# Optimization experiments

Hardware: AMD Instinct MI355X
Metric: run time of the kernel (lower is better)

The kernel has to match this reference:

```python
import jax, jax.numpy as jnp
import numpy as np
from jax.scipy.special import logsumexp

B, P, C, NOBJ = 32, 16384, 80, 50
THRESH = 0.5
NEGPOS = 3
VAR0, VAR1 = 0.1, 0.2


def setup_inputs() -> dict:
    key = jax.random.key(0)
    k1, k2, k3, k4, k5, k6, k7, k8 = jax.random.split(key, 8)
    loc_data = jax.random.normal(k1, (B, P, 4), dtype=jnp.float32)
    conf_data = jax.random.normal(k2, (B, P, C), dtype=jnp.float32)
    obj_data = jax.random.normal(k3, (B, P, 2), dtype=jnp.float32)
    # priors in (cx, cy, w, h) form, all in (0,1)
    cxcy = jax.random.uniform(k4, (P, 2), dtype=jnp.float32)
    wh = 0.05 + 0.45 * jax.random.uniform(k5, (P, 2), dtype=jnp.float32)
    priors = jnp.concatenate([cxcy, wh], axis=1)
    # targets: [xmin, ymin, xmax, ymax, label(1..C), weight]
    xy1 = 0.75 * jax.random.uniform(k6, (B, NOBJ, 2), dtype=jnp.float32)
    bwh = 0.02 + 0.23 * jax.random.uniform(k7, (B, NOBJ, 2), dtype=jnp.float32)
    lab = jax.random.randint(k8, (B, NOBJ, 1), 1, C + 1).astype(jnp.float32)
    wgt = 0.5 + 0.5 * jax.random.uniform(jax.random.fold_in(key, 99), (B, NOBJ, 1), dtype=jnp.float32)
    targets = jnp.concatenate([xy1, xy1 + bwh, lab, wgt], axis=-1)
    return {"loc_data": loc_data, "conf_data": conf_data, "obj_data": obj_data,
            "priors": priors, "targets": targets}


def point_form(p):
    return jnp.concatenate([p[:, :2] - p[:, 2:] / 2, p[:, :2] + p[:, 2:] / 2], axis=1)


def jaccard(a, b):  # a: [No,4] corner boxes, b: [Np,4] corner boxes
    lt = jnp.maximum(a[:, None, :2], b[None, :, :2])
    rb = jnp.minimum(a[:, None, 2:], b[None, :, 2:])
    wh = jnp.clip(rb - lt, 0.0)
    inter = wh[..., 0] * wh[..., 1]
    area_a = (a[:, 2] - a[:, 0]) * (a[:, 3] - a[:, 1])
    area_b = (b[:, 2] - b[:, 0]) * (b[:, 3] - b[:, 1])
    return inter / (area_a[:, None] + area_b[None, :] - inter)


def encode(matched, priors):
    g_cxcy = ((matched[:, :2] + matched[:, 2:]) / 2 - priors[:, :2]) / (VAR0 * priors[:, 2:])
    g_wh = jnp.log((matched[:, 2:] - matched[:, :2]) / priors[:, 2:]) / VAR1
    return jnp.concatenate([g_cxcy, g_wh], axis=1)


def match_one(truths, labels, priors):
    overlaps = jaccard(truths, point_form(priors))       # [No, Np]
    best_prior_idx = jnp.argmax(overlaps, axis=1)        # [No]
    best_truth_overlap = jnp.max(overlaps, axis=0)       # [Np]
    best_truth_idx = jnp.argmax(overlaps, axis=0)        # [Np]
    # ensure every GT keeps its best prior (overlap forced to 2)
    best_truth_overlap = best_truth_overlap.at[best_prior_idx].set(2.0)
    best_truth_idx = best_truth_idx.at[best_prior_idx].set(jnp.arange(truths.shape[0]))
    matched = truths[best_truth_idx]                     # [Np,4]
    lab = jnp.where(best_truth_overlap < THRESH, 0.0, labels[best_truth_idx, 0])
    w = labels[best_truth_idx, 1]
    loc = encode(matched, priors)
    return loc, jnp.stack([lab, w], axis=1), lab > 0


def _rank_desc(x):
    # rank of each entry in a descending per-row sort
    return jnp.argsort(jnp.argsort(-x, axis=1), axis=1)


def _ce(logits, tgt):
    return logsumexp(logits, axis=-1) - jnp.take_along_axis(logits, tgt[..., None], axis=-1)[..., 0]


def reference(loc_data, conf_data, obj_data, priors, targets):
    priors_c = jax.lax.stop_gradient(priors)
    targets_c = jax.lax.stop_gradient(targets)
    truths, labels = targets_c[:, :, :4], targets_c[:, :, 4:6]
    loc_t, conf_t, pos = jax.vmap(lambda t, l: match_one(t, l, priors_c))(truths, labels)
    nb, npri = pos.shape
    w = conf_t[:, :, 1]
    posf = pos.astype(loc_data.dtype)
    num_pos = (w * posf).sum(axis=1).astype(jnp.int32)           # weighted count, truncated
    num_neg = jnp.clip(NEGPOS * num_pos, None, npri - 1)

    # weighted smooth-L1 localization loss over positives
    d = loc_data - loc_t
    ad = jnp.abs(d)
    sl1 = jnp.where(ad < 1.0, 0.5 * d * d, ad - 0.5).sum(-1)     # [B,P]
    loss_l = jnp.sum(sl1 * w * posf)

    # combined objectness+class logits: [B,P,C+1]
    lse = logsumexp(conf_data, axis=-1, keepdims=True)
    logit = jnp.concatenate([obj_data[..., 0:1] + lse, obj_data[..., 1:2] + conf_data], axis=-1)
    tgt_c = conf_t[:, :, 0].astype(jnp.int32)
    ce_c = _ce(logit, tgt_c)                                     # [B,P]
    mine_c = jnp.where(pos, 0.0, jax.lax.stop_gradient(ce_c))
    neg_c = _rank_desc(mine_c) < num_neg[:, None]
    mask_c = pos | neg_c
    loss_c = jnp.sum(ce_c * w * mask_c)

    # objectness loss with its own hard-negative mining
    ce_o = _ce(obj_data, pos.astype(jnp.int32))
    mine_o = jnp.where(pos, 0.0, jax.lax.stop_gradient(ce_o))
    neg_o = _rank_desc(mine_o) < num_neg[:, None]
    mask_o = pos | neg_o
    loss_obj = jnp.sum(ce_o * w * mask_o)

    N = jnp.sum(w * posf)
    return loss_l / N, loss_c / N, loss_obj / N
```

## Files before the change

### kernel.cpp

```cpp
#include <hip/hip_runtime.h>
#include <cstdint>
#include <cstddef>

#define B_    32
#define P_    16384
#define C_    80
#define NOBJ_ 50
#define THRESH_ 0.5f

static constexpr size_t OFF_BP    = 1024;
static constexpr size_t OFF_MINEC = 16384;
static constexpr size_t SZ_BP32   = (size_t)B_ * P_ * 4;
static constexpr size_t OFF_MINEO = OFF_MINEC + SZ_BP32;
static constexpr size_t OFF_W     = OFF_MINEO + SZ_BP32;
static constexpr size_t OFF_POS   = OFF_W + SZ_BP32;
static constexpr size_t OFF_PMAIN = OFF_POS + (size_t)B_ * P_;
static constexpr size_t OFF_PSEL  = OFF_PMAIN + 2048 * 4 * 8;

__device__ __forceinline__ unsigned fkey(float f) {
    unsigned u = __float_as_uint(f);
    return (u & 0x80000000u) ? ~u : (u | 0x80000000u);
}

__device__ __forceinline__ void hist_add(unsigned bin, unsigned* hist) {
    int lane = threadIdx.x & 63;
    bool done = false;
    #pragma unroll
    for (int it = 0; it < 3; ++it) {
        unsigned long long active = __ballot(!done);
        if (!active) break;
        int leader = __ffsll((long long)active) - 1;
        unsigned lbin = __shfl(bin, leader);
        unsigned long long same = __ballot(!done && bin == lbin);
        if (!done && bin == lbin) {
            if (lane == leader) atomicAdd(&hist[bin], (unsigned)__popcll(same));
            done = true;
        }
    }
    if (!done) atomicAdd(&hist[bin], 1u);
}

__device__ double block_reduce_d(double v, double* sh, int nthreads) {
    int tid = threadIdx.x;
    sh[tid] = v; __syncthreads();
    for (int s = nthreads >> 1; s > 0; s >>= 1) {
        if (tid < s) sh[tid] += sh[tid + s];
        __syncthreads();
    }
    double r = sh[0]; __syncthreads();
    return r;
}

__global__ __launch_bounds__(256) void k_best_prior(
    const float* __restrict__ priors, const float* __restrict__ targets,
    int* __restrict__ bp)
{
    int t = blockIdx.x, b = blockIdx.y, tid = threadIdx.x;
    const float* tr = targets + (size_t)(b * NOBJ_ + t) * 6;
    float x1 = tr[0], y1 = tr[1], x2 = tr[2], y2 = tr[3];
    float areaA = (x2 - x1) * (y2 - y1);
    float best = -1.f; int bi = 0;
    for (int p = tid; p < P_; p += 256) {
        float4 pr = ((const float4*)priors)[p];
        float bx1 = pr.x - pr.z*0.5f, by1 = pr.y - pr.w*0.5f;
        float bx2 = pr.x + pr.z*0.5f, by2 = pr.y + pr.w*0.5f;
        float areaB = (bx2 - bx1) * (by2 - by1);
        float lx = fmaxf(x1, bx1), ly = fmaxf(y1, by1);
        float rx = fminf(x2, bx2), ry = fminf(y2, by2);
        float iw = fmaxf(rx - lx, 0.f), ih = fmaxf(ry - ly, 0.f);
        float inter = iw * ih;
        float iou = inter / (areaA + areaB - inter);
        if (iou > best) { best = iou; bi = p; }
    }
    __shared__ float sv[256];
    __shared__ int   si[256];
    sv[tid] = best; si[tid] = bi; __syncthreads();
    for (int s = 128; s > 0; s >>= 1) {
        if (tid < s) {
            if (sv[tid+s] > sv[tid] || (sv[tid+s] == sv[tid] && si[tid+s] < si[tid])) {
                sv[tid] = sv[tid+s]; si[tid] = si[tid+s];
            }
        }
        __syncthreads();
    }
    if (tid == 0) bp[b * NOBJ_ + t] = si[0];
}

__global__ __launch_bounds__(256) void k_main(
    const float* __restrict__ loc, const float* __restrict__ conf,
    const float* __restrict__ obj, const float* __restrict__ priors,
    const float* __restrict__ targets, const int* __restrict__ bp,
    float* __restrict__ mine_c, float* __restrict__ mine_o,
    float* __restrict__ wArr, uint8_t* __restrict__ posArr,
    double* __restrict__ pmain)
{
    int b = blockIdx.y;
    int row_base = blockIdx.x * 256;
    size_t base = (size_t)b * P_ + row_base;

    __shared__ float tg[NOBJ_ * 6];
    __shared__ float areaA[NOBJ_];
    __shared__ int   bpl[NOBJ_];
    __shared__ double wsum[4][4];
    for (int i = threadIdx.x; i < NOBJ_ * 6; i += 256) tg[i] = targets[(size_t)b * NOBJ_ * 6 + i];
    if (threadIdx.x < NOBJ_) bpl[threadIdx.x] = bp[b * NOBJ_ + threadIdx.x];
    __syncthreads();
    if (threadIdx.x < NOBJ_) {
        int t = threadIdx.x;
        areaA[t] = (tg[t*6+2] - tg[t*6+0]) * (tg[t*6+3] - tg[t*6+1]);
    }
    __syncthreads();

    int p = row_base + threadIdx.x;
    size_t ip = base + threadIdx.x;

    float4 prv = ((const float4*)priors)[p];
    float bx1 = prv.x - prv.z*0.5f, by1 = prv.y - prv.w*0.5f;
    float bx2 = prv.x + prv.z*0.5f, by2 = prv.y + prv.w*0.5f;
    float areaB = (bx2 - bx1) * (by2 - by1);
    float ov = -1.0f; int ti = 0;
    for (int t = 0; t < NOBJ_; ++t) {
        float lx = fmaxf(tg[t*6+0], bx1), ly = fmaxf(tg[t*6+1], by1);
        float rx = fminf(tg[t*6+2], bx2), ry = fminf(tg[t*6+3], by2);
        float iw = fmaxf(rx - lx, 0.f), ih = fmaxf(ry - ly, 0.f);
        float inter = iw * ih;
        float iou = inter / (areaA[t] + areaB - inter);
        if (iou > ov) { ov = iou; ti = t; }
    }
    for (int j = 0; j < NOBJ_; ++j) {
        if (bpl[j] == p) { ov = 2.0f; ti = j; }
    }

    float w  = tg[ti*6+5];
    bool pos = ov >= THRESH_;
    int  tgt = pos ? (int)tg[ti*6+4] : 0;

    float tx1 = tg[ti*6+0], ty1 = tg[ti*6+1], tx2 = tg[ti*6+2], ty2 = tg[ti*6+3];
    float gx = ((tx1 + tx2) * 0.5f - prv.x) / (0.1f * prv.z);
    float gy = ((ty1 + ty2) * 0.5f - prv.y) / (0.1f * prv.w);
    float gw = __logf((tx2 - tx1) / prv.z) * 5.0f;
    float gh = __logf((ty2 - ty1) / prv.w) * 5.0f;

    float4 l4 = ((const float4*)loc)[ip];
    float sl1 = 0.f;
    {
        float lrk[4] = {l4.x, l4.y, l4.z, l4.w};
        float g[4] = {gx, gy, gw, gh};
        #pragma unroll
        for (int k = 0; k < 4; ++k) {
            float d = lrk[k] - g[k];
            float ad = fabsf(d);
            sl1 += (ad < 1.0f) ? 0.5f * d * d : ad - 0.5f;
        }
    }

    float2 ob = ((const float2*)obj)[ip];
    float o0 = ob.x, o1 = ob.y;
    float mo = fmaxf(o0, o1);
    float lae = mo + __logf(__expf(o0 - mo) + __expf(o1 - mo));

    float ce_o = lae - (pos ? o1 : o0);
    float ce_c;
    if (tgt == 0) {
        ce_c = lae - o0;
    } else {
        const float4* cr = (const float4*)(conf + ip * C_);
        float m = -INFINITY;
        #pragma unroll 4
        for (int k = 0; k < C_/4; ++k) {
            float4 v = cr[k];
            m = fmaxf(m, fmaxf(fmaxf(v.x, v.y), fmaxf(v.z, v.w)));
        }
        float s = 0.f;
        #pragma unroll 4
        for (int k = 0; k < C_/4; ++k) {
            float4 v = cr[k];
            s += __expf(v.x - m) + __expf(v.y - m) + __expf(v.z - m) + __expf(v.w - m);
        }
        float lse = m + __logf(s);
        float ctgt = conf[ip * C_ + (tgt - 1)];
        ce_c = lse + lae - o1 - ctgt;
    }

    mine_c[ip] = pos ? 0.f : ce_c;
    mine_o[ip] = pos ? 0.f : ce_o;
    wArr[ip]   = w;
    posArr[ip] = pos ? 1 : 0;

    double v0 = pos ? (double)(sl1 * w)  : 0.0;
    double v1 = pos ? (double)(ce_c * w) : 0.0;
    double v2 = pos ? (double)(ce_o * w) : 0.0;
    double v3 = pos ? (double)w          : 0.0;

    #pragma unroll
    for (int d = 32; d; d >>= 1) {
        v0 += __shfl_xor(v0, d);
        v1 += __shfl_xor(v1, d);
        v2 += __shfl_xor(v2, d);
        v3 += __shfl_xor(v3, d);
    }
    int wid = threadIdx.x >> 6, lane = threadIdx.x & 63;
    if (lane == 0) { wsum[wid][0] = v0; wsum[wid][1] = v1; wsum[wid][2] = v2; wsum[wid][3] = v3; }
    __syncthreads();
    if (threadIdx.x == 0) {
        double t0 = 0, t1 = 0, t2 = 0, t3 = 0;
        #pragma unroll
        for (int i = 0; i < 4; ++i) { t0 += wsum[i][0]; t1 += wsum[i][1]; t2 += wsum[i][2]; t3 += wsum[i][3]; }
        size_t flat = (size_t)b * gridDim.x + blockIdx.x;
        pmain[flat*4+0] = t0; pmain[flat*4+1] = t1; pmain[flat*4+2] = t2; pmain[flat*4+3] = t3;
    }
}

#define SEL_T 1024
#define TIE_CAP 1024

__device__ __forceinline__ void suffix_scan_2048(unsigned* c, unsigned* wtot) {
    int tid = threadIdx.x;
    int lane = tid & 63, wid = tid >> 6;
    unsigned lo = c[2*tid], hi = c[2*tid+1];
    unsigned s_hi = hi;
    unsigned s_lo = lo + hi;
    unsigned tot = s_lo;
    unsigned run = tot;
    #pragma unroll
    for (int d = 1; d < 64; d <<= 1) {
        unsigned o = __shfl_down(run, d);
        if (lane + d < 64) run += o;
    }
    if (lane == 0) wtot[wid] = run;
    __syncthreads();
    unsigned woff = 0;
    #pragma unroll
    for (int w = 0; w < 16; ++w) if (w > wid) woff += wtot[w];
    unsigned base = woff + (run - tot);
    __syncthreads();
    c[2*tid]   = base + s_lo;
    c[2*tid+1] = base + s_hi;
    __syncthreads();
}

__device__ __forceinline__ void find_bin(unsigned* c, int K, int* s_bin, int* s_pre) {
    int tid = threadIdx.x;
    #pragma unroll
    for (int i = 0; i < 2; ++i) {
        int bb = tid + i * 1024;
        unsigned cb = c[bb];
        unsigned cn = (bb == 2047) ? 0u : c[bb + 1];
        if (cb >= (unsigned)K && cn < (unsigned)K) { *s_bin = bb; *s_pre = (int)cn; }
    }
    __syncthreads();
}

__global__ __launch_bounds__(SEL_T) void k_select(
    const float* __restrict__ mine_c, const float* __restrict__ mine_o,
    const float* __restrict__ wArr, const uint8_t* __restrict__ posArr,
    const double* __restrict__ pmain, double* __restrict__ psel)
{
    int b = blockIdx.x;
    int branch = blockIdx.y;
    int tid = threadIdx.x;

    __shared__ int sK;
    if (tid < 32) {
        double pn = pmain[(size_t)(b * 64 + tid) * 4 + 3]
                  + pmain[(size_t)(b * 64 + 32 + tid) * 4 + 3];
        #pragma unroll
        for (int d = 16; d; d >>= 1) pn += __shfl_xor(pn, d);
        if (tid == 0) {
            int np = (int)pn;
            int nn = 3 * np;
            sK = nn < (P_ - 1) ? nn : (P_ - 1);
        }
    }
    __syncthreads();
    int K = sK;
    if (K <= 0) { if (tid == 0) psel[branch * B_ + b] = 0.0; return; }

    const float* mrow = (branch ? mine_o : mine_c) + (size_t)b * P_;
    const float4* m4 = (const float4*)mrow;
    const float4* w4 = (const float4*)(wArr + (size_t)b * P_);
    const uchar4* p4 = (const uchar4*)(posArr + (size_t)b * P_);

    __shared__ unsigned hist[2048];
    __shared__ unsigned wtot[16];
    __shared__ int s_bin, s_pre;
    __shared__ int tcnt;
    __shared__ int tlist[TIE_CAP];
    __shared__ double rd[SEL_T];

    hist[tid] = 0; hist[tid + 1024] = 0;
    __syncthreads();
    for (int i = tid; i < P_/4; i += SEL_T) {
        float4 v = m4[i];
        hist_add(fkey(v.x) >> 21, hist);
        hist_add(fkey(v.y) >> 21, hist);
        hist_add(fkey(v.z) >> 21, hist);
        hist_add(fkey(v.w) >> 21, hist);
    }
    __syncthreads();
    suffix_scan_2048(hist, wtot);
    find_bin(hist, K, &s_bin, &s_pre);
    int bin1 = s_bin, pre1 = s_pre;
    __syncthreads();

    hist[tid] = 0; hist[tid + 1024] = 0;
    __syncthreads();
    for (int i = tid; i < P_/4; i += SEL_T) {
        float4 v = m4[i];
        unsigned k0 = fkey(v.x), k1 = fkey(v.y), k2 = fkey(v.z), k3 = fkey(v.w);
        if ((int)(k0 >> 21) == bin1) hist_add((k0 >> 10) & 0x7FFu, hist);
        if ((int)(k1 >> 21) == bin1) hist_add((k1 >> 10) & 0x7FFu, hist);
        if ((int)(k2 >> 21) == bin1) hist_add((k2 >> 10) & 0x7FFu, hist);
        if ((int)(k3 >> 21) == bin1) hist_add((k3 >> 10) & 0x7FFu, hist);
    }
    __syncthreads();
    suffix_scan_2048(hist, wtot);
    find_bin(hist, K - pre1, &s_bin, &s_pre);
    int bin2 = s_bin, pre2 = s_pre;
    __syncthreads();

    hist[tid] = 0; hist[tid + 1024] = 0;
    __syncthreads();
    unsigned hi21 = ((unsigned)bin1 << 11) | (unsigned)bin2;
    for (int i = tid; i < P_/4; i += SEL_T) {
        float4 v = m4[i];
        unsigned k0 = fkey(v.x), k1 = fkey(v.y), k2 = fkey(v.z), k3 = fkey(v.w);
        if ((k0 >> 10) == hi21) hist_add(k0 & 0x3FFu, hist);
        if ((k1 >> 10) == hi21) hist_add(k1 & 0x3FFu, hist);
        if ((k2 >> 10) == hi21) hist_add(k2 & 0x3FFu, hist);
        if ((k3 >> 10) == hi21) hist_add(k3 & 0x3FFu, hist);
    }
    __syncthreads();
    suffix_scan_2048(hist, wtot);
    find_bin(hist, K - pre1 - pre2, &s_bin, &s_pre);
    int bin3 = s_bin, pre3 = s_pre;
    __syncthreads();

    unsigned T = (hi21 << 10) | (unsigned)bin3;
    int mslots = K - (pre1 + pre2 + pre3);

    if (tid == 0) tcnt = 0;
    __syncthreads();
    double sum = 0.0;
    for (int i = tid; i < P_/4; i += SEL_T) {
        float4 v = m4[i];
        float4 wv = w4[i];
        uchar4 pv = p4[i];
        float  vv[4] = {v.x, v.y, v.z, v.w};
        float  ww[4] = {wv.x, wv.y, wv.z, wv.w};
        unsigned char pp[4] = {pv.x, pv.y, pv.z, pv.w};
        #pragma unroll
        for (int j = 0; j < 4; ++j) {
            unsigned k = fkey(vv[j]);
            if (k > T) {
                if (!pp[j]) sum += (double)vv[j] * (double)ww[j];
            } else if (k == T && !pp[j] && vv[j] != 0.0f) {
                int slot = atomicAdd(&tcnt, 1);
                if (slot < TIE_CAP) tlist[slot] = i * 4 + j;
            }
        }
    }
    __syncthreads();
    int n = tcnt < TIE_CAP ? tcnt : TIE_CAP;
    if (tid < n) {
        int myp = tlist[tid];
        bool sel;
        if (n <= mslots) {
            sel = true;
        } else {
            int r = 0;
            for (int j = 0; j < n; ++j) if (tlist[j] < myp) ++r;
            sel = (r < mslots);
        }
        if (sel) sum += (double)mrow[myp] * (double)(wArr + (size_t)b * P_)[myp];
    }
    double r = block_reduce_d(sum, rd, SEL_T);
    if (tid == 0) psel[branch * B_ + b] = r;
}

__global__ __launch_bounds__(1024) void k_final(
    const double* __restrict__ pmain, const double* __restrict__ psel,
    float* __restrict__ out)
{
    int tid = threadIdx.x;
    int lane = tid & 63, wid = tid >> 6;
    double s0 = 0, s1 = 0, s2 = 0, s3 = 0;
    for (int i = tid; i < 2048; i += 1024) {
        const double* pr = pmain + (size_t)i * 4;
        s0 += pr[0]; s1 += pr[1]; s2 += pr[2]; s3 += pr[3];
    }
    #pragma unroll
    for (int d = 32; d; d >>= 1) {
        s0 += __shfl_xor(s0, d); s1 += __shfl_xor(s1, d);
        s2 += __shfl_xor(s2, d); s3 += __shfl_xor(s3, d);
    }
    __shared__ double sh[16][4];
    if (lane == 0) { sh[wid][0] = s0; sh[wid][1] = s1; sh[wid][2] = s2; sh[wid][3] = s3; }
    __syncthreads();
    if (tid == 0) {
        double a0 = 0, a1 = 0, a2 = 0, N = 0;
        #pragma unroll
        for (int i = 0; i < 16; ++i) { a0 += sh[i][0]; a1 += sh[i][1]; a2 += sh[i][2]; N += sh[i][3]; }
        double selc = 0, selo = 0;
        for (int i = 0; i < B_; ++i) { selc += psel[i]; selo += psel[B_ + i]; }
        out[0] = (float)(a0 / N);
        out[1] = (float)((a1 + selc) / N);
        out[2] = (float)((a2 + selo) / N);
    }
}

extern "C" void kernel_launch(void* const* d_in, const int* in_sizes, int n_in,
                              void* d_out, int out_size, void* d_ws, size_t ws_size,
                              hipStream_t stream)
{
    const float* loc     = (const float*)d_in[0];
    const float* conf    = (const float*)d_in[1];
    const float* obj     = (const float*)d_in[2];
    const float* priors  = (const float*)d_in[3];
    const float* targets = (const float*)d_in[4];
    float* out = (float*)d_out;

    char* ws = (char*)d_ws;
    int*     bp     = (int*)(ws + OFF_BP);
    float*   mine_c = (float*)(ws + OFF_MINEC);
    float*   mine_o = (float*)(ws + OFF_MINEO);
    float*   wArr   = (float*)(ws + OFF_W);
    uint8_t* posArr = (uint8_t*)(ws + OFF_POS);
    double*  pmain  = (double*)(ws + OFF_PMAIN);
    double*  psel   = (double*)(ws + OFF_PSEL);

    k_best_prior <<<dim3(NOBJ_, B_), 256, 0, stream>>>(priors, targets, bp);
    k_main       <<<dim3(P_/256, B_), 256, 0, stream>>>(loc, conf, obj, priors, targets,
                                                        bp, mine_c, mine_o, wArr, posArr, pmain);
    k_select     <<<dim3(B_, 2), SEL_T, 0, stream>>>(mine_c, mine_o, wArr, posArr, pmain, psel);
    k_final      <<<1, 1024, 0, stream>>>(pmain, psel, out);
}
```

Measured before the change: 101.5 us.

## Share hard-negative mining across class and objectness losses and pack pos into weight sign

For non-positive priors the combined class cross-entropy reduces algebraically to the objectness cross-entropy (lae - o0), so a single selection pass now serves both losses. That pass recomputes the mining values on the fly from obj_data instead of reading stored mine_c and mine_o arrays. The main kernel writes one signed weight array, with the sign carrying the positive flag, in place of four per-prior arrays, cutting global write traffic and halving the selection grid. IoU divisions are replaced by cross-multiplied comparisons, which can shift tie-breaking and threshold decisions slightly at floating-point boundaries.

```diff
diff --git a/kernel.cpp b/kernel.cpp
--- a/kernel.cpp
+++ b/kernel.cpp
@@ -6,15 +6,11 @@
 #define P_    16384
 #define C_    80
 #define NOBJ_ 50
-#define THRESH_ 0.5f
 
 static constexpr size_t OFF_BP    = 1024;
-static constexpr size_t OFF_MINEC = 16384;
+static constexpr size_t OFF_WP    = 16384;
 static constexpr size_t SZ_BP32   = (size_t)B_ * P_ * 4;
-static constexpr size_t OFF_MINEO = OFF_MINEC + SZ_BP32;
-static constexpr size_t OFF_W     = OFF_MINEO + SZ_BP32;
-static constexpr size_t OFF_POS   = OFF_W + SZ_BP32;
-static constexpr size_t OFF_PMAIN = OFF_POS + (size_t)B_ * P_;
+static constexpr size_t OFF_PMAIN = OFF_WP + SZ_BP32;
 static constexpr size_t OFF_PSEL  = OFF_PMAIN + 2048 * 4 * 8;
 
 __device__ __forceinline__ unsigned fkey(float f) {
@@ -59,7 +55,7 @@
     const float* tr = targets + (size_t)(b * NOBJ_ + t) * 6;
     float x1 = tr[0], y1 = tr[1], x2 = tr[2], y2 = tr[3];
     float areaA = (x2 - x1) * (y2 - y1);
-    float best = -1.f; int bi = 0;
+    float bn = -1.f, bd = 1.f; int bi = 0;
     for (int p = tid; p < P_; p += 256) {
         float4 pr = ((const float4*)priors)[p];
         float bx1 = pr.x - pr.z*0.5f, by1 = pr.y - pr.w*0.5f;
@@ -69,16 +65,17 @@
         float rx = fminf(x2, bx2), ry = fminf(y2, by2);
         float iw = fmaxf(rx - lx, 0.f), ih = fmaxf(ry - ly, 0.f);
         float inter = iw * ih;
-        float iou = inter / (areaA + areaB - inter);
-        if (iou > best) { best = iou; bi = p; }
-    }
-    __shared__ float sv[256];
+        float uni = areaA + areaB - inter;
+        if (inter * bd > bn * uni) { bn = inter; bd = uni; bi = p; }
+    }
+    __shared__ float sn[256], sd[256];
     __shared__ int   si[256];
-    sv[tid] = best; si[tid] = bi; __syncthreads();
+    sn[tid] = bn; sd[tid] = bd; si[tid] = bi; __syncthreads();
     for (int s = 128; s > 0; s >>= 1) {
         if (tid < s) {
-            if (sv[tid+s] > sv[tid] || (sv[tid+s] == sv[tid] && si[tid+s] < si[tid])) {
-                sv[tid] = sv[tid+s]; si[tid] = si[tid+s];
+            float lhs = sn[tid+s] * sd[tid], rhs = sn[tid] * sd[tid+s];
+            if (lhs > rhs || (lhs == rhs && si[tid+s] < si[tid])) {
+                sn[tid] = sn[tid+s]; sd[tid] = sd[tid+s]; si[tid] = si[tid+s];
             }
         }
         __syncthreads();
@@ -90,9 +87,7 @@
     const float* __restrict__ loc, const float* __restrict__ conf,
     const float* __restrict__ obj, const float* __restrict__ priors,
     const float* __restrict__ targets, const int* __restrict__ bp,
-    float* __restrict__ mine_c, float* __restrict__ mine_o,
-    float* __restrict__ wArr, uint8_t* __restrict__ posArr,
-    double* __restrict__ pmain)
+    float* __restrict__ wp, double* __restrict__ pmain)
 {
     int b = blockIdx.y;
     int row_base = blockIdx.x * 256;
@@ -118,21 +113,21 @@
     float bx1 = prv.x - prv.z*0.5f, by1 = prv.y - prv.w*0.5f;
     float bx2 = prv.x + prv.z*0.5f, by2 = prv.y + prv.w*0.5f;
     float areaB = (bx2 - bx1) * (by2 - by1);
-    float ov = -1.0f; int ti = 0;
+    float bn = -1.f, bd = 1.f; int ti = 0;
     for (int t = 0; t < NOBJ_; ++t) {
         float lx = fmaxf(tg[t*6+0], bx1), ly = fmaxf(tg[t*6+1], by1);
         float rx = fminf(tg[t*6+2], bx2), ry = fminf(tg[t*6+3], by2);
         float iw = fmaxf(rx - lx, 0.f), ih = fmaxf(ry - ly, 0.f);
         float inter = iw * ih;
-        float iou = inter / (areaA[t] + areaB - inter);
-        if (iou > ov) { ov = iou; ti = t; }
-    }
+        float uni = areaA[t] + areaB - inter;
+        if (inter * bd > bn * uni) { bn = inter; bd = uni; ti = t; }
+    }
+    bool pos = (2.0f * bn >= bd);
     for (int j = 0; j < NOBJ_; ++j) {
-        if (bpl[j] == p) { ov = 2.0f; ti = j; }
+        if (bpl[j] == p) { pos = true; ti = j; }
     }
 
     float w  = tg[ti*6+5];
-    bool pos = ov >= THRESH_;
     int  tgt = pos ? (int)tg[ti*6+4] : 0;
 
     float tx1 = tg[ti*6+0], ty1 = tg[ti*6+1], tx2 = tg[ti*6+2], ty2 = tg[ti*6+3];
@@ -182,10 +177,7 @@
         ce_c = lse + lae - o1 - ctgt;
     }
 
-    mine_c[ip] = pos ? 0.f : ce_c;
-    mine_o[ip] = pos ? 0.f : ce_o;
-    wArr[ip]   = w;
-    posArr[ip] = pos ? 1 : 0;
+    wp[ip] = pos ? -w : w;
 
     double v0 = pos ? (double)(sl1 * w)  : 0.0;
     double v1 = pos ? (double)(ce_c * w) : 0.0;
@@ -252,12 +244,10 @@
 }
 
 __global__ __launch_bounds__(SEL_T) void k_select(
-    const float* __restrict__ mine_c, const float* __restrict__ mine_o,
-    const float* __restrict__ wArr, const uint8_t* __restrict__ posArr,
+    const float* __restrict__ obj, const float* __restrict__ wp,
     const double* __restrict__ pmain, double* __restrict__ psel)
 {
     int b = blockIdx.x;
-    int branch = blockIdx.y;
     int tid = threadIdx.x;
 
     __shared__ int sK;
@@ -274,12 +264,10 @@
     }
     __syncthreads();
     int K = sK;
-    if (K <= 0) { if (tid == 0) psel[branch * B_ + b] = 0.0; return; }
-
-    const float* mrow = (branch ? mine_o : mine_c) + (size_t)b * P_;
-    const float4* m4 = (const float4*)mrow;
-    const float4* w4 = (const float4*)(wArr + (size_t)b * P_);
-    const uchar4* p4 = (const uchar4*)(posArr + (size_t)b * P_);
+    if (K <= 0) { if (tid == 0) psel[b] = 0.0; return; }
+
+    const float2* o2 = (const float2*)(obj + (size_t)b * P_ * 2);
+    const float*  wr = wp + (size_t)b * P_;
 
     __shared__ unsigned hist[2048];
     __shared__ unsigned wtot[16];
@@ -288,14 +276,22 @@
     __shared__ int tlist[TIE_CAP];
     __shared__ double rd[SEL_T];
 
+    #define KEY_AT(i, kvar, vvar)                                          \
+        {                                                                  \
+            float2 _o = o2[i];                                             \
+            float _m = fmaxf(_o.x, _o.y);                                  \
+            float _lae = _m + __logf(__expf(_o.x - _m) + __expf(_o.y - _m));\
+            vvar = _lae - _o.x;                                            \
+            if (wr[i] < 0.f) vvar = 0.f;                                   \
+            kvar = fkey(vvar);                                             \
+        }
+
     hist[tid] = 0; hist[tid + 1024] = 0;
     __syncthreads();
-    for (int i = tid; i < P_/4; i += SEL_T) {
-        float4 v = m4[i];
-        hist_add(fkey(v.x) >> 21, hist);
-        hist_add(fkey(v.y) >> 21, hist);
-        hist_add(fkey(v.z) >> 21, hist);
-        hist_add(fkey(v.w) >> 21, hist);
+    for (int i = tid; i < P_; i += SEL_T) {
+        unsigned k; float v;
+        KEY_AT(i, k, v);
+        hist_add(k >> 21, hist);
     }
     __syncthreads();
     suffix_scan_2048(hist, wtot);
@@ -305,13 +301,10 @@
 
     hist[tid] = 0; hist[tid + 1024] = 0;
     __syncthreads();
-    for (int i = tid; i < P_/4; i += SEL_T) {
-        float4 v = m4[i];
-        unsigned k0 = fkey(v.x), k1 = fkey(v.y), k2 = fkey(v.z), k3 = fkey(v.w);
-        if ((int)(k0 >> 21) == bin1) hist_add((k0 >> 10) & 0x7FFu, hist);
-        if ((int)(k1 >> 21) == bin1) hist_add((k1 >> 10) & 0x7FFu, hist);
-        if ((int)(k2 >> 21) == bin1) hist_add((k2 >> 10) & 0x7FFu, hist);
-        if ((int)(k3 >> 21) == bin1) hist_add((k3 >> 10) & 0x7FFu, hist);
+    for (int i = tid; i < P_; i += SEL_T) {
+        unsigned k; float v;
+        KEY_AT(i, k, v);
+        if ((int)(k >> 21) == bin1) hist_add((k >> 10) & 0x7FFu, hist);
     }
     __syncthreads();
     suffix_scan_2048(hist, wtot);
@@ -322,13 +315,10 @@
     hist[tid] = 0; hist[tid + 1024] = 0;
     __syncthreads();
     unsigned hi21 = ((unsigned)bin1 << 11) | (unsigned)bin2;
-    for (int i = tid; i < P_/4; i += SEL_T) {
-        float4 v = m4[i];
-        unsigned k0 = fkey(v.x), k1 = fkey(v.y), k2 = fkey(v.z), k3 = fkey(v.w);
-        if ((k0 >> 10) == hi21) hist_add(k0 & 0x3FFu, hist);
-        if ((k1 >> 10) == hi21) hist_add(k1 & 0x3FFu, hist);
-        if ((k2 >> 10) == hi21) hist_add(k2 & 0x3FFu, hist);
-        if ((k3 >> 10) == hi21) hist_add(k3 & 0x3FFu, hist);
+    for (int i = tid; i < P_; i += SEL_T) {
+        unsigned k; float v;
+        KEY_AT(i, k, v);
+        if ((k >> 10) == hi21) hist_add(k & 0x3FFu, hist);
     }
     __syncthreads();
     suffix_scan_2048(hist, wtot);
@@ -342,22 +332,16 @@
     if (tid == 0) tcnt = 0;
     __syncthreads();
     double sum = 0.0;
-    for (int i = tid; i < P_/4; i += SEL_T) {
-        float4 v = m4[i];
-        float4 wv = w4[i];
-        uchar4 pv = p4[i];
-        float  vv[4] = {v.x, v.y, v.z, v.w};
-        float  ww[4] = {wv.x, wv.y, wv.z, wv.w};
-        unsigned char pp[4] = {pv.x, pv.y, pv.z, pv.w};
-        #pragma unroll
-        for (int j = 0; j < 4; ++j) {
-            unsigned k = fkey(vv[j]);
-            if (k > T) {
-                if (!pp[j]) sum += (double)vv[j] * (double)ww[j];
-            } else if (k == T && !pp[j] && vv[j] != 0.0f) {
-                int slot = atomicAdd(&tcnt, 1);
-                if (slot < TIE_CAP) tlist[slot] = i * 4 + j;
-            }
+    for (int i = tid; i < P_; i += SEL_T) {
+        unsigned k; float v;
+        KEY_AT(i, k, v);
+        float w = wr[i];
+        bool neg = (w >= 0.f);
+        if (k > T) {
+            if (neg) sum += (double)v * (double)w;
+        } else if (k == T && neg && v != 0.0f) {
+            int slot = atomicAdd(&tcnt, 1);
+            if (slot < TIE_CAP) tlist[slot] = i;
         }
     }
     __syncthreads();
@@ -372,10 +356,15 @@
             for (int j = 0; j < n; ++j) if (tlist[j] < myp) ++r;
             sel = (r < mslots);
         }
-        if (sel) sum += (double)mrow[myp] * (double)(wArr + (size_t)b * P_)[myp];
-    }
+        if (sel) {
+            unsigned k; float v;
+            KEY_AT(myp, k, v);
+            sum += (double)v * (double)wr[myp];
+        }
+    }
+    #undef KEY_AT
     double r = block_reduce_d(sum, rd, SEL_T);
-    if (tid == 0) psel[branch * B_ + b] = r;
+    if (tid == 0) psel[b] = r;
 }
 
 __global__ __launch_bounds__(1024) void k_final(
@@ -401,11 +390,11 @@
         double a0 = 0, a1 = 0, a2 = 0, N = 0;
         #pragma unroll
         for (int i = 0; i < 16; ++i) { a0 += sh[i][0]; a1 += sh[i][1]; a2 += sh[i][2]; N += sh[i][3]; }
-        double selc = 0, selo = 0;
-        for (int i = 0; i < B_; ++i) { selc += psel[i]; selo += psel[B_ + i]; }
+        double sel = 0;
+        for (int i = 0; i < B_; ++i) sel += psel[i];
         out[0] = (float)(a0 / N);
-        out[1] = (float)((a1 + selc) / N);
-        out[2] = (float)((a2 + selo) / N);
+        out[1] = (float)((a1 + sel) / N);
+        out[2] = (float)((a2 + sel) / N);
     }
 }
 
@@ -421,17 +410,14 @@
     float* out = (float*)d_out;
 
     char* ws = (char*)d_ws;
-    int*     bp     = (int*)(ws + OFF_BP);
-    float*   mine_c = (float*)(ws + OFF_MINEC);
-    float*   mine_o = (float*)(ws + OFF_MINEO);
-    float*   wArr   = (float*)(ws + OFF_W);
-    uint8_t* posArr = (uint8_t*)(ws + OFF_POS);
-    double*  pmain  = (double*)(ws + OFF_PMAIN);
-    double*  psel   = (double*)(ws + OFF_PSEL);
+    int*    bp    = (int*)(ws + OFF_BP);
+    float*  wpArr = (float*)(ws + OFF_WP);
+    double* pmain = (double*)(ws + OFF_PMAIN);
+    double* psel  = (double*)(ws + OFF_PSEL);
 
     k_best_prior <<<dim3(NOBJ_, B_), 256, 0, stream>>>(priors, targets, bp);
     k_main       <<<dim3(P_/256, B_), 256, 0, stream>>>(loc, conf, obj, priors, targets,
-                                                        bp, mine_c, mine_o, wArr, posArr, pmain);
-    k_select     <<<dim3(B_, 2), SEL_T, 0, stream>>>(mine_c, mine_o, wArr, posArr, pmain, psel);
+                                                        bp, wpArr, pmain);
+    k_select     <<<B_, SEL_T, 0, stream>>>(obj, wpArr, pmain, psel);
     k_final      <<<1, 1024, 0, stream>>>(pmain, psel, out);
 }
```

New measurement: 101.9 us. About the same (+0.4%).
